# Kernel optimization log

Hardware: AMD Instinct MI355X
Metric: run time of the kernel (lower is better)

## Reference

```python
import jax, jax.numpy as jnp
import numpy as np

# ---- static config (mirrors init_kwargs) ----
NS, NV, ORDER = 16, 4, 1
NUM_RBF, NUM_CH = 8, 4
C = NUM_RBF * NUM_CH              # 32 output channels per l in out_irreps
N_NODES, N_EDGES = 10000, 128000
NODE_FEAT, EDGE_FEAT = 64, 16
RDIM, RMAX = 32, 12.0
L, FC_DIM = 2, 64
# FullyConnectedTensorProduct weight numel for order=1 paths:
# (0x0->0), (0x1->1), (1x0->1), (1x1->0), (1x1->1)
WNUM = NS*NS + NS*NV + NV*NV + NV*NS + NV*NV  # 416


def _get_sorter(order, nc):
    # faithful port of TensorProductConvModel.get_sorter
    idx, orl = [], []
    for l in range(order + 1):
        for n in range(nc):
            idx.extend([n] * (2 * l + 1))
            orl.extend(range(l * l, (l + 1) * (l + 1)))
    idx, orl = np.array(idx), np.array(orl)
    return np.argsort(idx * (orl.max() + 1) + orl, kind='stable')

SORTER = jnp.asarray(_get_sorter(ORDER, C))


def _mlp(x, W1, b1, W2, b2):
    return jnp.maximum(x @ W1 + b1, 0.0) @ W2 + b2


def setup_inputs() -> dict:
    key = jax.random.key(0)
    ks = jax.random.split(key, 24)
    rn = lambda k, sh, sc: jax.random.normal(k, sh, dtype=jnp.float32) * sc
    s = lambda f: 1.0 / np.sqrt(f)
    inp = {}
    inp['pos'] = rn(ks[0], (N_NODES, 3), 3.0)
    inp['node_feats'] = rn(ks[1], (N_NODES, NODE_FEAT), 1.0)
    inp['edge_attr_in'] = rn(ks[2], (N_EDGES, EDGE_FEAT), 1.0)
    inp['edge_index'] = jax.random.randint(ks[3], (2, N_EDGES), 0, N_NODES)
    # Encoder (linear) + node_embedding MLP
    inp['enc_W'] = rn(ks[4], (NODE_FEAT, NS), s(NODE_FEAT)); inp['enc_b'] = jnp.zeros((NS,), jnp.float32)
    inp['ne_W1'] = rn(ks[5], (NS, NS), s(NS)); inp['ne_b1'] = jnp.zeros((NS,), jnp.float32)
    inp['ne_W2'] = rn(ks[6], (NS, NS), s(NS)); inp['ne_b2'] = jnp.zeros((NS,), jnp.float32)
    # edge_embedding MLP
    inp['ee_W1'] = rn(ks[7], (EDGE_FEAT, NS), s(EDGE_FEAT)); inp['ee_b1'] = jnp.zeros((NS,), jnp.float32)
    inp['ee_W2'] = rn(ks[8], (NS, NS), s(NS)); inp['ee_b2'] = jnp.zeros((NS,), jnp.float32)
    # radius_embedding MLP
    inp['re_W1'] = rn(ks[9], (RDIM, NS), s(RDIM)); inp['re_b1'] = jnp.zeros((NS,), jnp.float32)
    inp['re_W2'] = rn(ks[10], (NS, NS), s(NS)); inp['re_b2'] = jnp.zeros((NS,), jnp.float32)
    # per-layer TP edge-weight MLPs (stacked over L layers)
    inp['fc1_W'] = rn(ks[11], (L, 3 * NS, FC_DIM), s(3 * NS)); inp['fc1_b'] = jnp.zeros((L, FC_DIM), jnp.float32)
    inp['fc2_W'] = rn(ks[12], (L, FC_DIM, WNUM), s(FC_DIM)); inp['fc2_b'] = jnp.zeros((L, WNUM), jnp.float32)
    # final o3.Linear (per-l channel mixing)
    inp['lin0_W'] = rn(ks[13], (NS, C), 1.0)
    inp['lin1_W'] = rn(ks[14], (NV, C), 1.0)
    return inp


def _forward(pos, node_feats, edge_attr_in, enc_W, enc_b, ne_W1, ne_b1, ne_W2, ne_b2,
             ee_W1, ee_b1, ee_W2, ee_b2, re_W1, re_b1, re_W2, re_b2,
             fc1_W, fc1_b, fc2_W, fc2_b, lin0_W, lin1_W, edge_index):
    src, dst = edge_index[0], edge_index[1]
    N, E = pos.shape[0], src.shape[0]
    # node scalar features: Encoder -> node_embedding MLP
    h0 = _mlp(node_feats @ enc_W + enc_b, ne_W1, ne_b1, ne_W2, ne_b2)        # [N, ns]
    h1 = jnp.zeros((N, NV, 3), h0.dtype)                                      # l=1 part (zero-padded)
    # build_conv_graph (radius=False): given edges only
    edge_vec = pos[src] - pos[dst]                                            # [E, 3]
    d = jnp.linalg.norm(edge_vec, axis=-1)
    offset = jnp.linspace(0.0, RMAX, RDIM)
    coeff = -0.5 / (offset[1] - offset[0]) ** 2
    rbf = jnp.exp(coeff * (d[:, None] - offset[None, :]) ** 2)                # GaussianSmearing
    edge_attr = _mlp(edge_attr_in, ee_W1, ee_b1, ee_W2, ee_b2) + _mlp(rbf, re_W1, re_b1, re_W2, re_b2)
    # spherical harmonics, normalize=True, component normalization: Y0=1, Y1=sqrt(3)*unit
    unit = edge_vec / jnp.maximum(d, 1e-9)[:, None]
    y1 = jnp.sqrt(3.0) * unit                                                 # [E, 3]
    # scatter-mean denominators (dim_size = N)
    cnt = jnp.maximum(jax.ops.segment_sum(jnp.ones((E,), h0.dtype), src, num_segments=N), 1.0)
    a0 = 1.0 / jnp.sqrt(float(NS + NV))       # path (fan-in) norm for l=0 output
    a1 = 1.0 / jnp.sqrt(float(NS + 2 * NV))   # path norm for l=1 output
    for i in range(L):
        # edge features: [edge_attr | h0[src] | h0[dst]] -> per-edge TP weights
        ea = jnp.concatenate([edge_attr, h0[src], h0[dst]], -1)
        w = _mlp(ea, fc1_W[i], fc1_b[i], fc2_W[i], fc2_b[i])                  # [E, WNUM]
        off = 0
        w00 = w[:, off:off + NS * NS].reshape(E, NS, NS); off += NS * NS
        w011 = w[:, off:off + NS * NV].reshape(E, NS, NV); off += NS * NV
        w101 = w[:, off:off + NV * NV].reshape(E, NV, NV); off += NV * NV
        w110 = w[:, off:off + NV * NS].reshape(E, NV, NS); off += NV * NS
        w111 = w[:, off:off + NV * NV].reshape(E, NV, NV)
        x0, x1 = h0[dst], h1[dst]                                             # gather at edge_dst
        # l=0 output: (0x0->0) + (1x1->0)
        dot = jnp.einsum('enk,ek->en', x1, y1) / jnp.sqrt(3.0)
        o0 = a0 * (jnp.einsum('en,eno->eo', x0, w00) + jnp.einsum('en,eno->eo', dot, w110))
        # l=1 output: (0x1->1) + (1x0->1) + (1x1->1 cross)
        cr = jnp.cross(x1, y1[:, None, :]) / jnp.sqrt(2.0)                    # [E, nv, 3]
        o1 = a1 * (jnp.einsum('en,eno,em->eom', x0, w011, y1)
                   + jnp.einsum('enm,eno->eom', x1, w101)
                   + jnp.einsum('enm,eno->eom', cr, w111))
        # scatter-mean into edge_src, residual add
        h0 = h0 + jax.ops.segment_sum(o0, src, num_segments=N) / cnt[:, None]
        h1 = h1 + jax.ops.segment_sum(o1.reshape(E, -1), src, num_segments=N).reshape(N, NV, 3) / cnt[:, None, None]
    # final o3.Linear (per-l, fan-in normalized) -> sorter -> reshape
    f0 = (h0 @ lin0_W) / jnp.sqrt(float(NS))                                   # [N, C]
    f1 = jnp.einsum('nvm,vc->ncm', h1, lin1_W) / jnp.sqrt(float(NV))           # [N, C, 3]
    flat = jnp.concatenate([f0, f1.reshape(N, C * 3)], -1)                     # irreps-flat layout
    return flat[:, SORTER].reshape(N, NUM_CH, NUM_RBF, (ORDER + 1) ** 2)


def reference(pos, node_feats, edge_attr_in, edge_index, enc_W, enc_b, ne_W1, ne_b1, ne_W2, ne_b2,
              ee_W1, ee_b1, ee_W2, ee_b2, re_W1, re_b1, re_W2, re_b2,
              fc1_W, fc1_b, fc2_W, fc2_b, lin0_W, lin1_W):
    return _forward(pos, node_feats, edge_attr_in, enc_W, enc_b, ne_W1, ne_b1, ne_W2, ne_b2,
                    ee_W1, ee_b1, ee_W2, ee_b2, re_W1, re_b1, re_W2, re_b2,
                    fc1_W, fc1_b, fc2_W, fc2_b, lin0_W, lin1_W, edge_index)
```

## Files before the change

kernel.cpp:

```cpp
#include <hip/hip_runtime.h>
#include <math.h>

#define SQRT3f     1.7320508075688772f
#define INV_SQRT3f 0.5773502691896258f
#define INV_SQRT2f 0.7071067811865476f
#define A0f        0.22360679774997896f
#define A1f        0.20412414523193150f

typedef __attribute__((ext_vector_type(8))) short bf16x8;
typedef __attribute__((ext_vector_type(4))) float f32x4;

__device__ __forceinline__ float4 ld4(const float* p) {
    return *reinterpret_cast<const float4*>(p);
}

__device__ __forceinline__ unsigned short f2bf(float x) {
    unsigned int u = __float_as_uint(x);
    u = (u + 0x7FFFu + ((u >> 16) & 1u)) >> 16;
    return (unsigned short)u;
}
__device__ __forceinline__ float bf2f(unsigned short u) {
    return __uint_as_float(((unsigned int)u) << 16);
}
__device__ __forceinline__ unsigned int pk2(float a, float b) {
    return (unsigned int)f2bf(a) | ((unsigned int)f2bf(b) << 16);
}

template<bool RELU>
__device__ __forceinline__ void mm16x16(const float* in, const float* W,
                                        const float* b, float* out)
{
#pragma unroll
    for (int t = 0; t < 16; ++t) out[t] = b[t];
#pragma unroll
    for (int s = 0; s < 16; ++s) {
        float a = in[s];
#pragma unroll
        for (int q = 0; q < 4; ++q) {
            float4 w = *reinterpret_cast<const float4*>(W + s * 16 + q * 4);
            out[q*4+0] += a * w.x; out[q*4+1] += a * w.y;
            out[q*4+2] += a * w.z; out[q*4+3] += a * w.w;
        }
    }
    if (RELU) {
#pragma unroll
        for (int t = 0; t < 16; ++t) out[t] = fmaxf(out[t], 0.f);
    }
}

__global__ __launch_bounds__(256)
void node_embed_kernel(const float* __restrict__ nf,
                       const float* __restrict__ encW, const float* __restrict__ encb,
                       const float* __restrict__ neW1, const float* __restrict__ neb1,
                       const float* __restrict__ neW2, const float* __restrict__ neb2,
                       float* __restrict__ h0, int N)
{
    int n = blockIdx.x * blockDim.x + threadIdx.x;
    if (n >= N) return;
    float x[16];
#pragma unroll
    for (int s = 0; s < 16; ++s) x[s] = encb[s];
    for (int i = 0; i < 64; ++i) {
        float a = nf[n * 64 + i];
#pragma unroll
        for (int q = 0; q < 4; ++q) {
            float4 w = ld4(encW + i * 16 + q * 4);
            x[q*4+0] += a * w.x; x[q*4+1] += a * w.y;
            x[q*4+2] += a * w.z; x[q*4+3] += a * w.w;
        }
    }
    float h[16], o[16];
    mm16x16<true >(x, neW1, neb1, h);
    mm16x16<false>(h, neW2, neb2, o);
#pragma unroll
    for (int j = 0; j < 16; ++j) h0[n * 16 + j] = o[j];
}

__global__ __launch_bounds__(256)
void hist_kernel(const int* __restrict__ srcI, int* __restrict__ cntI, int E)
{
    int e = blockIdx.x * blockDim.x + threadIdx.x;
    if (e < E) atomicAdd(&cntI[srcI[e]], 1);
}

__global__ __launch_bounds__(1024)
void scan_kernel(const int* __restrict__ cntI, int* __restrict__ start,
                 int* __restrict__ cursor, float* __restrict__ invcnt, int N)
{
    __shared__ int sd[1024];
    int tid = threadIdx.x;
    int run = 0;
    for (int c0 = 0; c0 < N; c0 += 1024) {
        int i = c0 + tid;
        int v = (i < N) ? cntI[i] : 0;
        sd[tid] = v;
        __syncthreads();
        for (int s = 1; s < 1024; s <<= 1) {
            int t = (tid >= s) ? sd[tid - s] : 0;
            __syncthreads();
            sd[tid] += t;
            __syncthreads();
        }
        int incl = sd[tid];
        int total = sd[1023];
        if (i < N) {
            int st = run + incl - v;
            start[i] = st;
            cursor[i] = st;
            invcnt[i] = 1.0f / fmaxf((float)v, 1.0f);
        }
        run += total;
        __syncthreads();
    }
}

__global__ __launch_bounds__(256)
void perm_kernel(const int* __restrict__ srcI, int* __restrict__ cursor,
                 int* __restrict__ perm, int E)
{
    int e = blockIdx.x * blockDim.x + threadIdx.x;
    if (e >= E) return;
    int p = atomicAdd(&cursor[srcI[e]], 1);
    perm[p] = e;
}

__global__ __launch_bounds__(256)
void edge_pre_kernel(const float* __restrict__ pos, const float* __restrict__ eain,
                     const int* __restrict__ srcI, const int* __restrict__ dstI,
                     const int* __restrict__ perm,
                     const float* __restrict__ eeW1, const float* __restrict__ eeb1,
                     const float* __restrict__ eeW2, const float* __restrict__ eeb2,
                     const float* __restrict__ reW1, const float* __restrict__ reb1,
                     const float* __restrict__ reW2, const float* __restrict__ reb2,
                     float* __restrict__ eattr, float* __restrict__ y1s,
                     int* __restrict__ srcS, int* __restrict__ dstS, int E)
{
    __shared__ float ws_[256 + 256 + 512 + 256];
    __shared__ float bs_[64];
    float* eeW1s = ws_;
    float* eeW2s = ws_ + 256;
    float* reW1s = ws_ + 512;
    float* reW2s = ws_ + 1024;
    int tid = threadIdx.x;
    if (tid < 256) eeW1s[tid] = eeW1[tid];
    if (tid < 256) eeW2s[tid] = eeW2[tid];
    for (int i = tid; i < 512; i += 256) reW1s[i] = reW1[i];
    if (tid < 256) reW2s[tid] = reW2[tid];
    if (tid < 16) bs_[tid]      = eeb1[tid];
    if (tid >= 16 && tid < 32)  bs_[tid] = eeb2[tid - 16];
    if (tid >= 32 && tid < 48)  bs_[tid] = reb1[tid - 32];
    if (tid >= 48 && tid < 64)  bs_[tid] = reb2[tid - 48];
    __syncthreads();

    int p = blockIdx.x * blockDim.x + tid;
    if (p >= E) return;
    int e = perm[p];
    int s = srcI[e], d = dstI[e];
    srcS[p] = s; dstS[p] = d;
    float vx = pos[s*3+0] - pos[d*3+0];
    float vy = pos[s*3+1] - pos[d*3+1];
    float vz = pos[s*3+2] - pos[d*3+2];
    float dist = sqrtf(vx*vx + vy*vy + vz*vz);
    float inv = 1.f / fmaxf(dist, 1e-9f);
    y1s[p*3+0] = SQRT3f * vx * inv;
    y1s[p*3+1] = SQRT3f * vy * inv;
    y1s[p*3+2] = SQRT3f * vz * inv;

    const float step  = 12.0f / 31.0f;
    const float coeff = -0.5f / (step * step);
    float rbf[32];
#pragma unroll
    for (int j = 0; j < 32; ++j) {
        float t = dist - (float)j * step;
        rbf[j] = expf(coeff * t * t);
    }

    float ein[16];
#pragma unroll
    for (int j = 0; j < 16; ++j) ein[j] = eain[(size_t)e * 16 + j];

    float t1[16], a1v[16];
    mm16x16<true >(ein, eeW1s, bs_, t1);
    mm16x16<false>(t1, eeW2s, bs_ + 16, a1v);

    float t2[16];
#pragma unroll
    for (int t = 0; t < 16; ++t) t2[t] = bs_[32 + t];
#pragma unroll
    for (int j = 0; j < 32; ++j) {
        float a = rbf[j];
#pragma unroll
        for (int q = 0; q < 4; ++q) {
            float4 w = *reinterpret_cast<const float4*>(&reW1s[j * 16 + q * 4]);
            t2[q*4+0] += a * w.x; t2[q*4+1] += a * w.y;
            t2[q*4+2] += a * w.z; t2[q*4+3] += a * w.w;
        }
    }
#pragma unroll
    for (int t = 0; t < 16; ++t) t2[t] = fmaxf(t2[t], 0.f);
    float a2v[16];
    mm16x16<false>(t2, reW2s, bs_ + 48, a2v);

#pragma unroll
    for (int j = 0; j < 16; ++j) eattr[(size_t)p * 16 + j] = a1v[j] + a2v[j];
}

__global__ void pack_w2_kernel(const float* __restrict__ fc2W, unsigned short* __restrict__ w2p)
{
    int idx = blockIdx.x * blockDim.x + threadIdx.x;
    if (idx >= 2 * 26 * 2 * 64) return;
    int lane  = idx & 63;
    int ks    = (idx >> 6) & 1;
    int nt    = (idx >> 7) % 26;
    int layer = idx / (26 * 2 * 64);
    const float* W = fc2W + (size_t)layer * 64 * 416;
    unsigned short* out = w2p + (size_t)layer * 26 * 2 * 64 * 8
                              + (size_t)((nt * 2 + ks) * 64 + lane) * 8;
    int k0 = ks * 32 + (lane >> 4) * 8;
    int c  = nt * 16 + (lane & 15);
#pragma unroll
    for (int j = 0; j < 8; ++j) out[j] = f2bf(W[(size_t)(k0 + j) * 416 + c]);
}

__global__ void pack_w1_kernel(const float* __restrict__ fc1W, unsigned short* __restrict__ w1p)
{
    int idx = blockIdx.x * blockDim.x + threadIdx.x;
    if (idx >= 2 * 4 * 2 * 64) return;
    int lane  = idx & 63;
    int ks    = (idx >> 6) & 1;
    int nt    = (idx >> 7) & 3;
    int layer = idx >> 9;
    const float* W = fc1W + (size_t)layer * 48 * 64;
    unsigned short* out = w1p + (size_t)(((layer * 4 + nt) * 2 + ks) * 64 + lane) * 8;
    int k0 = ks * 32 + (lane >> 4) * 8;
    int n  = nt * 16 + (lane & 15);
#pragma unroll
    for (int j = 0; j < 8; ++j) {
        int k = k0 + j;
        out[j] = (k < 48) ? f2bf(W[(size_t)k * 64 + n]) : (unsigned short)0;
    }
}

template<bool HAS_L1>
__global__ __launch_bounds__(256)
void fused_tp_kernel(const float* __restrict__ h0, const float* __restrict__ h1,
                     const float* __restrict__ eattr, const float* __restrict__ y1s,
                     const int* __restrict__ srcS, const int* __restrict__ dstS,
                     const unsigned short* __restrict__ w1p, const float* __restrict__ b1,
                     const unsigned short* __restrict__ w2p, const float* __restrict__ b2,
                     float* __restrict__ oo0, float* __restrict__ oo1, int E)
{
    __shared__ unsigned short eas[128 * 64];
    __shared__ unsigned short x0s[128 * 18];
    __shared__ unsigned short x1s[128 * 14];
    __shared__ unsigned short dots[128 * 6];
    __shared__ unsigned short crs[128 * 14];
    __shared__ unsigned short y1l[128 * 6];

    int tid = threadIdx.x;
    int ebase = blockIdx.x * 128;

    {
        int lx = tid & 127;
        int half = tid >> 7;
        int p = ebase + lx;
        int sw = lx & 7;
        uint4 pk;
        if (half == 0) {
            float4 va = ld4(eattr + (size_t)p * 16 + 0);
            float4 vb = ld4(eattr + (size_t)p * 16 + 4);
            float4 vc = ld4(eattr + (size_t)p * 16 + 8);
            float4 vd = ld4(eattr + (size_t)p * 16 + 12);
            pk.x = pk2(va.x, va.y); pk.y = pk2(va.z, va.w);
            pk.z = pk2(vb.x, vb.y); pk.w = pk2(vb.z, vb.w);
            *reinterpret_cast<uint4*>(&eas[lx * 64 + ((0 ^ sw) << 3)]) = pk;
            pk.x = pk2(vc.x, vc.y); pk.y = pk2(vc.z, vc.w);
            pk.z = pk2(vd.x, vd.y); pk.w = pk2(vd.z, vd.w);
            *reinterpret_cast<uint4*>(&eas[lx * 64 + ((1 ^ sw) << 3)]) = pk;

            int s = srcS[p];
            va = ld4(h0 + (size_t)s * 16 + 0); vb = ld4(h0 + (size_t)s * 16 + 4);
            vc = ld4(h0 + (size_t)s * 16 + 8); vd = ld4(h0 + (size_t)s * 16 + 12);
            pk.x = pk2(va.x, va.y); pk.y = pk2(va.z, va.w);
            pk.z = pk2(vb.x, vb.y); pk.w = pk2(vb.z, vb.w);
            *reinterpret_cast<uint4*>(&eas[lx * 64 + ((2 ^ sw) << 3)]) = pk;
            pk.x = pk2(vc.x, vc.y); pk.y = pk2(vc.z, vc.w);
            pk.z = pk2(vd.x, vd.y); pk.w = pk2(vd.z, vd.w);
            *reinterpret_cast<uint4*>(&eas[lx * 64 + ((3 ^ sw) << 3)]) = pk;
        } else {
            int d = dstS[p];
            float4 va = ld4(h0 + (size_t)d * 16 + 0);
            float4 vb = ld4(h0 + (size_t)d * 16 + 4);
            float4 vc = ld4(h0 + (size_t)d * 16 + 8);
            float4 vd = ld4(h0 + (size_t)d * 16 + 12);
            pk.x = pk2(va.x, va.y); pk.y = pk2(va.z, va.w);
            pk.z = pk2(vb.x, vb.y); pk.w = pk2(vb.z, vb.w);
            *reinterpret_cast<uint4*>(&eas[lx * 64 + ((4 ^ sw) << 3)]) = pk;
            pk.x = pk2(vc.x, vc.y); pk.y = pk2(vc.z, vc.w);
            pk.z = pk2(vd.x, vd.y); pk.w = pk2(vd.z, vd.w);
            *reinterpret_cast<uint4*>(&eas[lx * 64 + ((5 ^ sw) << 3)]) = pk;
            uint4 z = {0u, 0u, 0u, 0u};
            *reinterpret_cast<uint4*>(&eas[lx * 64 + ((6 ^ sw) << 3)]) = z;
            *reinterpret_cast<uint4*>(&eas[lx * 64 + ((7 ^ sw) << 3)]) = z;

            x0s[lx*18+ 0]=f2bf(va.x); x0s[lx*18+ 1]=f2bf(va.y);
            x0s[lx*18+ 2]=f2bf(va.z); x0s[lx*18+ 3]=f2bf(va.w);
            x0s[lx*18+ 4]=f2bf(vb.x); x0s[lx*18+ 5]=f2bf(vb.y);
            x0s[lx*18+ 6]=f2bf(vb.z); x0s[lx*18+ 7]=f2bf(vb.w);
            x0s[lx*18+ 8]=f2bf(vc.x); x0s[lx*18+ 9]=f2bf(vc.y);
            x0s[lx*18+10]=f2bf(vc.z); x0s[lx*18+11]=f2bf(vc.w);
            x0s[lx*18+12]=f2bf(vd.x); x0s[lx*18+13]=f2bf(vd.y);
            x0s[lx*18+14]=f2bf(vd.z); x0s[lx*18+15]=f2bf(vd.w);

            float yv0 = y1s[(size_t)p*3+0], yv1 = y1s[(size_t)p*3+1], yv2 = y1s[(size_t)p*3+2];
            y1l[lx*6+0] = f2bf(yv0); y1l[lx*6+1] = f2bf(yv1); y1l[lx*6+2] = f2bf(yv2);

            if (HAS_L1) {
#pragma unroll
                for (int v = 0; v < 4; ++v) {
                    float xa = h1[(size_t)d*12 + v*3 + 0];
                    float xb = h1[(size_t)d*12 + v*3 + 1];
                    float xc = h1[(size_t)d*12 + v*3 + 2];
                    x1s[lx*14 + v*3 + 0] = f2bf(xa);
                    x1s[lx*14 + v*3 + 1] = f2bf(xb);
                    x1s[lx*14 + v*3 + 2] = f2bf(xc);
                    dots[lx*6 + v] = f2bf((xa*yv0 + xb*yv1 + xc*yv2) * INV_SQRT3f);
                    crs[lx*14 + v*3 + 0] = f2bf((xb*yv2 - xc*yv1) * INV_SQRT2f);
                    crs[lx*14 + v*3 + 1] = f2bf((xc*yv0 - xa*yv2) * INV_SQRT2f);
                    crs[lx*14 + v*3 + 2] = f2bf((xa*yv1 - xb*yv0) * INV_SQRT2f);
                }
            }
        }
    }
    __syncthreads();

    int wave = tid >> 6;
    int lane = tid & 63;
    int col = lane & 15;
    int grp = lane >> 4;
    int mrow0 = wave * 32;

    {
        bf16x8 a1[2][2];
#pragma unroll
        for (int m = 0; m < 2; ++m) {
            int row = mrow0 + m * 16 + col;
            int r7 = row & 7;
#pragma unroll
            for (int ks = 0; ks < 2; ++ks) {
                int kc = grp + ks * 4;
                a1[m][ks] = *reinterpret_cast<const bf16x8*>(
                    &eas[row * 64 + ((kc ^ r7) << 3)]);
            }
        }
        f32x4 hacc[4][2];
#pragma unroll
        for (int nt = 0; nt < 4; ++nt) {
            const bf16x8* bp = reinterpret_cast<const bf16x8*>(
                w1p + (size_t)((nt * 2) * 64 + lane) * 8);
            bf16x8 b0 = bp[0];
            bf16x8 b1f = bp[64];
            float bs = b1[nt * 16 + col];
            f32x4 cin = {bs, bs, bs, bs};
#pragma unroll
            for (int m = 0; m < 2; ++m) {
                f32x4 acc = cin;
                acc = __builtin_amdgcn_mfma_f32_16x16x32_bf16(a1[m][0], b0, acc, 0, 0, 0);
                acc = __builtin_amdgcn_mfma_f32_16x16x32_bf16(a1[m][1], b1f, acc, 0, 0, 0);
                hacc[nt][m] = acc;
            }
        }
#pragma unroll
        for (int nt = 0; nt < 4; ++nt) {
            int chunkbase = nt * 2 + (col >> 3);
            int cw = col & 7;
#pragma unroll
            for (int m = 0; m < 2; ++m) {
#pragma unroll
                for (int r = 0; r < 4; ++r) {
                    int edge = mrow0 + m * 16 + grp * 4 + r;
                    unsigned short hv = f2bf(fmaxf(hacc[nt][m][r], 0.f));
                    eas[edge * 64 + ((chunkbase ^ (edge & 7)) << 3) + cw] = hv;
                }
            }
        }
    }

    asm volatile("s_waitcnt lgkmcnt(0)" ::: "memory");
    __builtin_amdgcn_sched_barrier(0);

    bf16x8 a[2][2];
#pragma unroll
    for (int m = 0; m < 2; ++m) {
        int row = mrow0 + m * 16 + col;
        int r7 = row & 7;
        a[m][0] = *reinterpret_cast<const bf16x8*>(&eas[row * 64 + ((grp ^ r7) << 3)]);
        a[m][1] = *reinterpret_cast<const bf16x8*>(&eas[row * 64 + (((grp + 4) ^ r7) << 3)]);
    }

    float o0a[2][4];
    float t011p[2][4];
    float o1p[2][4][3];
#pragma unroll
    for (int m = 0; m < 2; ++m)
#pragma unroll
        for (int r = 0; r < 4; ++r) {
            o0a[m][r] = 0.f; t011p[m][r] = 0.f;
            o1p[m][r][0] = 0.f; o1p[m][r][1] = 0.f; o1p[m][r][2] = 0.f;
        }

    const int NT = HAS_L1 ? 26 : 20;
    for (int nt = 0; nt < NT; ++nt) {
        const bf16x8* bp = reinterpret_cast<const bf16x8*>(
            w2p + (size_t)(nt * 2 * 64 + lane) * 8);
        bf16x8 b0 = bp[0];
        bf16x8 b1f = bp[64];
        float bias = b2[nt * 16 + col];
        f32x4 cin = {bias, bias, bias, bias};
#pragma unroll
        for (int m = 0; m < 2; ++m) {
            f32x4 acc = cin;
            acc = __builtin_amdgcn_mfma_f32_16x16x32_bf16(a[m][0], b0, acc, 0, 0, 0);
            acc = __builtin_amdgcn_mfma_f32_16x16x32_bf16(a[m][1], b1f, acc, 0, 0, 0);
            int lx0 = mrow0 + m * 16 + grp * 4;
            if (nt < 16) {
#pragma unroll
                for (int r = 0; r < 4; ++r)
                    o0a[m][r] += bf2f(x0s[(lx0 + r) * 18 + nt]) * acc[r];
            } else if (nt < 20) {
                int n = (nt - 16) * 4 + (col >> 2);
#pragma unroll
                for (int r = 0; r < 4; ++r)
                    t011p[m][r] += bf2f(x0s[(lx0 + r) * 18 + n]) * acc[r];
            } else if (nt == 20) {
                int n = col >> 2;
#pragma unroll
                for (int r = 0; r < 4; ++r) {
#pragma unroll
                    for (int d = 0; d < 3; ++d)
                        o1p[m][r][d] += bf2f(x1s[(lx0 + r) * 14 + n * 3 + d]) * acc[r];
                }
            } else if (nt < 25) {
                int n = nt - 21;
#pragma unroll
                for (int r = 0; r < 4; ++r)
                    o0a[m][r] += bf2f(dots[(lx0 + r) * 6 + n]) * acc[r];
            } else {
                int n = col >> 2;
#pragma unroll
                for (int r = 0; r < 4; ++r) {
#pragma unroll
                    for (int d = 0; d < 3; ++d)
                        o1p[m][r][d] += bf2f(crs[(lx0 + r) * 14 + n * 3 + d]) * acc[r];
                }
            }
        }
    }

#pragma unroll
    for (int m = 0; m < 2; ++m) {
        int lx0 = mrow0 + m * 16 + grp * 4;
#pragma unroll
        for (int r = 0; r < 4; ++r) {
            int lx = lx0 + r;
            size_t e = (size_t)(ebase + lx);
            float t = t011p[m][r];
            t += __shfl_xor(t, 4);
            t += __shfl_xor(t, 8);
            float o1v[3];
#pragma unroll
            for (int d = 0; d < 3; ++d) {
                float v = o1p[m][r][d];
                v += __shfl_xor(v, 4);
                v += __shfl_xor(v, 8);
                o1v[d] = v + t * bf2f(y1l[lx * 6 + d]);
            }
            oo0[e * 16 + col] = A0f * o0a[m][r];
            if (col < 4) {
#pragma unroll
                for (int d = 0; d < 3; ++d)
                    oo1[e * 12 + col * 3 + d] = A1f * o1v[d];
            }
        }
    }
}

__global__ void node_update_kernel(float* __restrict__ h0, float* __restrict__ h1,
                                   const float* __restrict__ oo0, const float* __restrict__ oo1,
                                   const int* __restrict__ start, const int* __restrict__ cntI,
                                   const float* __restrict__ invcnt, int N)
{
    int j = threadIdx.x;
    int n = blockIdx.x * blockDim.y + threadIdx.y;
    if (n >= N || j >= 28) return;
    int p0 = start[n], p1 = p0 + cntI[n];
    float acc = 0.f;
    if (j < 16) {
        for (int p = p0; p < p1; ++p) acc += oo0[(size_t)p * 16 + j];
        h0[(size_t)n * 16 + j] += acc * invcnt[n];
    } else {
        int m = j - 16;
        for (int p = p0; p < p1; ++p) acc += oo1[(size_t)p * 12 + m];
        h1[(size_t)n * 12 + m] += acc * invcnt[n];
    }
}

__global__ __launch_bounds__(256)
void final_kernel(const float* __restrict__ h0, const float* __restrict__ h1,
                  const float* __restrict__ lin0, const float* __restrict__ lin1,
                  float* __restrict__ out, int N)
{
    int i = blockIdx.x * blockDim.x + threadIdx.x;
    if (i >= N * 32) return;
    int n = i >> 5, c = i & 31;
    float f0 = 0.f;
#pragma unroll
    for (int s = 0; s < 16; ++s) f0 += h0[n * 16 + s] * lin0[s * 32 + c];
    f0 *= 0.25f;
    float f1x = 0.f, f1y = 0.f, f1z = 0.f;
#pragma unroll
    for (int v = 0; v < 4; ++v) {
        float w = lin1[v * 32 + c];
        f1x += h1[n * 12 + v * 3 + 0] * w;
        f1y += h1[n * 12 + v * 3 + 1] * w;
        f1z += h1[n * 12 + v * 3 + 2] * w;
    }
    float4 r;
    r.x = f0;
    r.y = f1x * 0.5f;
    r.z = f1y * 0.5f;
    r.w = f1z * 0.5f;
    *reinterpret_cast<float4*>(out + (size_t)n * 128 + c * 4) = r;
}

extern "C" void kernel_launch(void* const* d_in, const int* in_sizes, int n_in,
                              void* d_out, int out_size, void* d_ws, size_t ws_size,
                              hipStream_t stream)
{
    const float* pos  = (const float*)d_in[0];
    const float* nf   = (const float*)d_in[1];
    const float* eain = (const float*)d_in[2];
    const int*   eidx = (const int*)  d_in[3];
    const float* encW = (const float*)d_in[4];
    const float* encb = (const float*)d_in[5];
    const float* neW1 = (const float*)d_in[6];
    const float* neb1 = (const float*)d_in[7];
    const float* neW2 = (const float*)d_in[8];
    const float* neb2 = (const float*)d_in[9];
    const float* eeW1 = (const float*)d_in[10];
    const float* eeb1 = (const float*)d_in[11];
    const float* eeW2 = (const float*)d_in[12];
    const float* eeb2 = (const float*)d_in[13];
    const float* reW1 = (const float*)d_in[14];
    const float* reb1 = (const float*)d_in[15];
    const float* reW2 = (const float*)d_in[16];
    const float* reb2 = (const float*)d_in[17];
    const float* fc1W = (const float*)d_in[18];
    const float* fc1b = (const float*)d_in[19];
    const float* fc2W = (const float*)d_in[20];
    const float* fc2b = (const float*)d_in[21];
    const float* lin0 = (const float*)d_in[22];
    const float* lin1 = (const float*)d_in[23];

    int N = in_sizes[0] / 3;
    int E = in_sizes[3] / 2;
    const int* srcI = eidx;
    const int* dstI = eidx + E;

    float* ws = (float*)d_ws;
    size_t o = 0;
    float* h0     = ws + o; o += (size_t)N * 16;
    float* h1     = ws + o; o += (size_t)N * 12;
    float* eat    = ws + o; o += (size_t)E * 16;
    float* y1s    = ws + o; o += (size_t)E * 3;
    float* oo0    = ws + o; o += (size_t)E * 16;
    float* oo1    = ws + o; o += (size_t)E * 12;
    float* invcnt = ws + o; o += (size_t)N;
    int* cntI   = (int*)(ws + o); o += (size_t)N;
    int* startA = (int*)(ws + o); o += (size_t)N;
    int* cursor = (int*)(ws + o); o += (size_t)N;
    int* perm   = (int*)(ws + o); o += (size_t)E;
    int* srcS   = (int*)(ws + o); o += (size_t)E;
    int* dstS   = (int*)(ws + o); o += (size_t)E;
    unsigned short* w2p = (unsigned short*)(ws + o); o += 2 * 26 * 2 * 64 * 8 / 2;
    unsigned short* w1p = (unsigned short*)(ws + o); o += 2 * 4 * 2 * 64 * 8 / 2;

    hipMemsetAsync(h1,   0, sizeof(float) * (size_t)N * 12, stream);
    hipMemsetAsync(cntI, 0, sizeof(int) * (size_t)N, stream);

    pack_w2_kernel<<<26, 256, 0, stream>>>(fc2W, w2p);
    pack_w1_kernel<<<4, 256, 0, stream>>>(fc1W, w1p);
    node_embed_kernel<<<(N + 255) / 256, 256, 0, stream>>>(
        nf, encW, encb, neW1, neb1, neW2, neb2, h0, N);

    hist_kernel<<<(E + 255) / 256, 256, 0, stream>>>(srcI, cntI, E);
    scan_kernel<<<1, 1024, 0, stream>>>(cntI, startA, cursor, invcnt, N);
    perm_kernel<<<(E + 255) / 256, 256, 0, stream>>>(srcI, cursor, perm, E);

    edge_pre_kernel<<<(E + 255) / 256, 256, 0, stream>>>(
        pos, eain, srcI, dstI, perm, eeW1, eeb1, eeW2, eeb2,
        reW1, reb1, reW2, reb2, eat, y1s, srcS, dstS, E);

    for (int i = 0; i < 2; ++i) {
        const float* fb1 = fc1b + (size_t)i * 64;
        const float* fb2 = fc2b + (size_t)i * 416;
        const unsigned short* w1pi = w1p + (size_t)i * 4 * 2 * 64 * 8;
        const unsigned short* w2pi = w2p + (size_t)i * 26 * 2 * 64 * 8;
        if (i == 0) {
            fused_tp_kernel<false><<<E / 128, 256, 0, stream>>>(
                h0, h1, eat, y1s, srcS, dstS, w1pi, fb1, w2pi, fb2, oo0, oo1, E);
        } else {
            fused_tp_kernel<true><<<E / 128, 256, 0, stream>>>(
                h0, h1, eat, y1s, srcS, dstS, w1pi, fb1, w2pi, fb2, oo0, oo1, E);
        }
        dim3 blk(32, 8);
        node_update_kernel<<<(N + 7) / 8, blk, 0, stream>>>(
            h0, h1, oo0, oo1, startA, cntI, invcnt, N);
    }

    final_kernel<<<((size_t)N * 32 + 255) / 256, 256, 0, stream>>>(
        h0, h1, lin0, lin1, (float*)d_out, N);
}
```

Baseline: 287.6 us.

## Fuse embed with histogram, perm into edge_pre, and final linear into node update

Merges several small launches: the node embedding and the edge histogram share one grid, both weight-pack kernels become one, the permutation kernel is folded into edge_pre via an atomic cursor, and the final linear is fused into the last node-update pass. The scan is replaced with wave shuffles, and node update now reads float4 vectors and stages weights in shared memory. This cuts launch count and the perm array traffic. In exchange the edge order within each segment becomes nondeterministic, and edge_pre now reads in original edge order.

Result: faster. 265.3 us (-7.8%).

```diff
diff --git a/kernel.cpp b/kernel.cpp
--- a/kernel.cpp
+++ b/kernel.cpp
@@ -49,85 +49,101 @@
 }
 
 __global__ __launch_bounds__(256)
-void node_embed_kernel(const float* __restrict__ nf,
+void embed_hist_kernel(const float* __restrict__ nf,
                        const float* __restrict__ encW, const float* __restrict__ encb,
                        const float* __restrict__ neW1, const float* __restrict__ neb1,
                        const float* __restrict__ neW2, const float* __restrict__ neb2,
-                       float* __restrict__ h0, int N)
-{
-    int n = blockIdx.x * blockDim.x + threadIdx.x;
+                       float* __restrict__ h0, int N,
+                       const int* __restrict__ srcI, int* __restrict__ cntI, int E,
+                       int nblkA)
+{
+    int tid = threadIdx.x;
+    if ((int)blockIdx.x >= nblkA) {
+        int e = ((int)blockIdx.x - nblkA) * 256 + tid;
+        if (e < E) atomicAdd(&cntI[srcI[e]], 1);
+        return;
+    }
+    __shared__ float encWs[1024];
+    __shared__ float neW1s[256];
+    __shared__ float neW2s[256];
+    __shared__ float bs[48];
+    for (int i = tid; i < 1024; i += 256) encWs[i] = encW[i];
+    neW1s[tid] = neW1[tid];
+    neW2s[tid] = neW2[tid];
+    if (tid < 16)      bs[tid] = encb[tid];
+    else if (tid < 32) bs[tid] = neb1[tid - 16];
+    else if (tid < 48) bs[tid] = neb2[tid - 32];
+    __syncthreads();
+
+    int n = blockIdx.x * 256 + tid;
     if (n >= N) return;
     float x[16];
 #pragma unroll
-    for (int s = 0; s < 16; ++s) x[s] = encb[s];
+    for (int s = 0; s < 16; ++s) x[s] = bs[s];
     for (int i = 0; i < 64; ++i) {
-        float a = nf[n * 64 + i];
+        float a = nf[(size_t)n * 64 + i];
 #pragma unroll
         for (int q = 0; q < 4; ++q) {
-            float4 w = ld4(encW + i * 16 + q * 4);
+            float4 w = *reinterpret_cast<const float4*>(&encWs[i * 16 + q * 4]);
             x[q*4+0] += a * w.x; x[q*4+1] += a * w.y;
             x[q*4+2] += a * w.z; x[q*4+3] += a * w.w;
         }
     }
     float h[16], o[16];
-    mm16x16<true >(x, neW1, neb1, h);
-    mm16x16<false>(h, neW2, neb2, o);
-#pragma unroll
-    for (int j = 0; j < 16; ++j) h0[n * 16 + j] = o[j];
-}
-
-__global__ __launch_bounds__(256)
-void hist_kernel(const int* __restrict__ srcI, int* __restrict__ cntI, int E)
-{
-    int e = blockIdx.x * blockDim.x + threadIdx.x;
-    if (e < E) atomicAdd(&cntI[srcI[e]], 1);
+    mm16x16<true >(x, neW1s, bs + 16, h);
+    mm16x16<false>(h, neW2s, bs + 32, o);
+#pragma unroll
+    for (int j = 0; j < 16; ++j) h0[(size_t)n * 16 + j] = o[j];
 }
 
 __global__ __launch_bounds__(1024)
 void scan_kernel(const int* __restrict__ cntI, int* __restrict__ start,
                  int* __restrict__ cursor, float* __restrict__ invcnt, int N)
 {
-    __shared__ int sd[1024];
+    __shared__ int wsum[16];
+    __shared__ int ctot;
     int tid = threadIdx.x;
+    int lane = tid & 63, wid = tid >> 6;
     int run = 0;
     for (int c0 = 0; c0 < N; c0 += 1024) {
         int i = c0 + tid;
         int v = (i < N) ? cntI[i] : 0;
-        sd[tid] = v;
+        int x = v;
+#pragma unroll
+        for (int off = 1; off < 64; off <<= 1) {
+            int y = __shfl_up(x, off);
+            if (lane >= off) x += y;
+        }
+        if (lane == 63) wsum[wid] = x;
         __syncthreads();
-        for (int s = 1; s < 1024; s <<= 1) {
-            int t = (tid >= s) ? sd[tid - s] : 0;
-            __syncthreads();
-            sd[tid] += t;
-            __syncthreads();
-        }
-        int incl = sd[tid];
-        int total = sd[1023];
+        if (wid == 0) {
+            int w = (lane < 16) ? wsum[lane] : 0;
+#pragma unroll
+            for (int off = 1; off < 16; off <<= 1) {
+                int y = __shfl_up(w, off);
+                if (lane >= off) w += y;
+            }
+            if (lane < 16) wsum[lane] = w;
+            if (lane == 15) ctot = w;
+        }
+        __syncthreads();
+        int base = (wid > 0) ? wsum[wid - 1] : 0;
+        int incl = x + base;
         if (i < N) {
             int st = run + incl - v;
             start[i] = st;
             cursor[i] = st;
             invcnt[i] = 1.0f / fmaxf((float)v, 1.0f);
         }
-        run += total;
+        run += ctot;
         __syncthreads();
     }
-}
-
-__global__ __launch_bounds__(256)
-void perm_kernel(const int* __restrict__ srcI, int* __restrict__ cursor,
-                 int* __restrict__ perm, int E)
-{
-    int e = blockIdx.x * blockDim.x + threadIdx.x;
-    if (e >= E) return;
-    int p = atomicAdd(&cursor[srcI[e]], 1);
-    perm[p] = e;
 }
 
 __global__ __launch_bounds__(256)
 void edge_pre_kernel(const float* __restrict__ pos, const float* __restrict__ eain,
                      const int* __restrict__ srcI, const int* __restrict__ dstI,
-                     const int* __restrict__ perm,
+                     int* __restrict__ cursor,
                      const float* __restrict__ eeW1, const float* __restrict__ eeb1,
                      const float* __restrict__ eeW2, const float* __restrict__ eeb2,
                      const float* __restrict__ reW1, const float* __restrict__ reb1,
@@ -135,36 +151,37 @@
                      float* __restrict__ eattr, float* __restrict__ y1s,
                      int* __restrict__ srcS, int* __restrict__ dstS, int E)
 {
-    __shared__ float ws_[256 + 256 + 512 + 256];
+    __shared__ float ws_[1280];
     __shared__ float bs_[64];
     float* eeW1s = ws_;
     float* eeW2s = ws_ + 256;
     float* reW1s = ws_ + 512;
     float* reW2s = ws_ + 1024;
     int tid = threadIdx.x;
-    if (tid < 256) eeW1s[tid] = eeW1[tid];
-    if (tid < 256) eeW2s[tid] = eeW2[tid];
-    for (int i = tid; i < 512; i += 256) reW1s[i] = reW1[i];
-    if (tid < 256) reW2s[tid] = reW2[tid];
-    if (tid < 16) bs_[tid]      = eeb1[tid];
-    if (tid >= 16 && tid < 32)  bs_[tid] = eeb2[tid - 16];
-    if (tid >= 32 && tid < 48)  bs_[tid] = reb1[tid - 32];
-    if (tid >= 48 && tid < 64)  bs_[tid] = reb2[tid - 48];
+    eeW1s[tid] = eeW1[tid];
+    eeW2s[tid] = eeW2[tid];
+    reW1s[tid] = reW1[tid];
+    reW1s[tid + 256] = reW1[tid + 256];
+    reW2s[tid] = reW2[tid];
+    if (tid < 16)      bs_[tid] = eeb1[tid];
+    else if (tid < 32) bs_[tid] = eeb2[tid - 16];
+    else if (tid < 48) bs_[tid] = reb1[tid - 32];
+    else if (tid < 64) bs_[tid] = reb2[tid - 48];
     __syncthreads();
 
-    int p = blockIdx.x * blockDim.x + tid;
-    if (p >= E) return;
-    int e = perm[p];
+    int e = blockIdx.x * blockDim.x + tid;
+    if (e >= E) return;
     int s = srcI[e], d = dstI[e];
+    int p = atomicAdd(&cursor[s], 1);
     srcS[p] = s; dstS[p] = d;
     float vx = pos[s*3+0] - pos[d*3+0];
     float vy = pos[s*3+1] - pos[d*3+1];
     float vz = pos[s*3+2] - pos[d*3+2];
     float dist = sqrtf(vx*vx + vy*vy + vz*vz);
     float inv = 1.f / fmaxf(dist, 1e-9f);
-    y1s[p*3+0] = SQRT3f * vx * inv;
-    y1s[p*3+1] = SQRT3f * vy * inv;
-    y1s[p*3+2] = SQRT3f * vz * inv;
+    y1s[(size_t)p*3+0] = SQRT3f * vx * inv;
+    y1s[(size_t)p*3+1] = SQRT3f * vy * inv;
+    y1s[(size_t)p*3+2] = SQRT3f * vz * inv;
 
     const float step  = 12.0f / 31.0f;
     const float coeff = -0.5f / (step * step);
@@ -205,39 +222,39 @@
     for (int j = 0; j < 16; ++j) eattr[(size_t)p * 16 + j] = a1v[j] + a2v[j];
 }
 
-__global__ void pack_w2_kernel(const float* __restrict__ fc2W, unsigned short* __restrict__ w2p)
+__global__ void pack_w_kernel(const float* __restrict__ fc2W, const float* __restrict__ fc1W,
+                              unsigned short* __restrict__ w2p, unsigned short* __restrict__ w1p)
 {
     int idx = blockIdx.x * blockDim.x + threadIdx.x;
-    if (idx >= 2 * 26 * 2 * 64) return;
-    int lane  = idx & 63;
-    int ks    = (idx >> 6) & 1;
-    int nt    = (idx >> 7) % 26;
-    int layer = idx / (26 * 2 * 64);
-    const float* W = fc2W + (size_t)layer * 64 * 416;
-    unsigned short* out = w2p + (size_t)layer * 26 * 2 * 64 * 8
-                              + (size_t)((nt * 2 + ks) * 64 + lane) * 8;
-    int k0 = ks * 32 + (lane >> 4) * 8;
-    int c  = nt * 16 + (lane & 15);
-#pragma unroll
-    for (int j = 0; j < 8; ++j) out[j] = f2bf(W[(size_t)(k0 + j) * 416 + c]);
-}
-
-__global__ void pack_w1_kernel(const float* __restrict__ fc1W, unsigned short* __restrict__ w1p)
-{
-    int idx = blockIdx.x * blockDim.x + threadIdx.x;
-    if (idx >= 2 * 4 * 2 * 64) return;
-    int lane  = idx & 63;
-    int ks    = (idx >> 6) & 1;
-    int nt    = (idx >> 7) & 3;
-    int layer = idx >> 9;
-    const float* W = fc1W + (size_t)layer * 48 * 64;
-    unsigned short* out = w1p + (size_t)(((layer * 4 + nt) * 2 + ks) * 64 + lane) * 8;
-    int k0 = ks * 32 + (lane >> 4) * 8;
-    int n  = nt * 16 + (lane & 15);
-#pragma unroll
-    for (int j = 0; j < 8; ++j) {
-        int k = k0 + j;
-        out[j] = (k < 48) ? f2bf(W[(size_t)k * 64 + n]) : (unsigned short)0;
+    const int NW2 = 2 * 26 * 2 * 64;
+    if (idx < NW2) {
+        int lane  = idx & 63;
+        int ks    = (idx >> 6) & 1;
+        int nt    = (idx >> 7) % 26;
+        int layer = idx / (26 * 2 * 64);
+        const float* W = fc2W + (size_t)layer * 64 * 416;
+        unsigned short* out = w2p + (size_t)layer * 26 * 2 * 64 * 8
+                                  + (size_t)((nt * 2 + ks) * 64 + lane) * 8;
+        int k0 = ks * 32 + (lane >> 4) * 8;
+        int c  = nt * 16 + (lane & 15);
+#pragma unroll
+        for (int j = 0; j < 8; ++j) out[j] = f2bf(W[(size_t)(k0 + j) * 416 + c]);
+    } else {
+        int i2 = idx - NW2;
+        if (i2 >= 2 * 4 * 2 * 64) return;
+        int lane  = i2 & 63;
+        int ks    = (i2 >> 6) & 1;
+        int nt    = (i2 >> 7) & 3;
+        int layer = i2 >> 9;
+        const float* W = fc1W + (size_t)layer * 48 * 64;
+        unsigned short* out = w1p + (size_t)(((layer * 4 + nt) * 2 + ks) * 64 + lane) * 8;
+        int k0 = ks * 32 + (lane >> 4) * 8;
+        int n  = nt * 16 + (lane & 15);
+#pragma unroll
+        for (int j = 0; j < 8; ++j) {
+            int k = k0 + j;
+            out[j] = (k < 48) ? f2bf(W[(size_t)k * 64 + n]) : (unsigned short)0;
+        }
     }
 }
 
@@ -485,52 +502,92 @@
     }
 }
 
-__global__ void node_update_kernel(float* __restrict__ h0, float* __restrict__ h1,
-                                   const float* __restrict__ oo0, const float* __restrict__ oo1,
-                                   const int* __restrict__ start, const int* __restrict__ cntI,
-                                   const float* __restrict__ invcnt, int N)
-{
-    int j = threadIdx.x;
-    int n = blockIdx.x * blockDim.y + threadIdx.y;
-    if (n >= N || j >= 28) return;
-    int p0 = start[n], p1 = p0 + cntI[n];
-    float acc = 0.f;
-    if (j < 16) {
-        for (int p = p0; p < p1; ++p) acc += oo0[(size_t)p * 16 + j];
-        h0[(size_t)n * 16 + j] += acc * invcnt[n];
-    } else {
-        int m = j - 16;
-        for (int p = p0; p < p1; ++p) acc += oo1[(size_t)p * 12 + m];
-        h1[(size_t)n * 12 + m] += acc * invcnt[n];
-    }
-}
-
+template<bool FINAL>
 __global__ __launch_bounds__(256)
-void final_kernel(const float* __restrict__ h0, const float* __restrict__ h1,
-                  const float* __restrict__ lin0, const float* __restrict__ lin1,
-                  float* __restrict__ out, int N)
-{
-    int i = blockIdx.x * blockDim.x + threadIdx.x;
-    if (i >= N * 32) return;
-    int n = i >> 5, c = i & 31;
-    float f0 = 0.f;
-#pragma unroll
-    for (int s = 0; s < 16; ++s) f0 += h0[n * 16 + s] * lin0[s * 32 + c];
-    f0 *= 0.25f;
-    float f1x = 0.f, f1y = 0.f, f1z = 0.f;
-#pragma unroll
-    for (int v = 0; v < 4; ++v) {
-        float w = lin1[v * 32 + c];
-        f1x += h1[n * 12 + v * 3 + 0] * w;
-        f1y += h1[n * 12 + v * 3 + 1] * w;
-        f1z += h1[n * 12 + v * 3 + 2] * w;
-    }
-    float4 r;
-    r.x = f0;
-    r.y = f1x * 0.5f;
-    r.z = f1y * 0.5f;
-    r.w = f1z * 0.5f;
-    *reinterpret_cast<float4*>(out + (size_t)n * 128 + c * 4) = r;
+void node_update_kernel(float* __restrict__ h0, float* __restrict__ h1,
+                        const float* __restrict__ oo0, const float* __restrict__ oo1,
+                        const int* __restrict__ start, const int* __restrict__ cntI,
+                        const float* __restrict__ invcnt,
+                        const float* __restrict__ lin0, const float* __restrict__ lin1,
+                        float* __restrict__ out, int N)
+{
+    __shared__ float lin0s[512];
+    __shared__ float lin1s[128];
+    __shared__ float hh0[32][16];
+    __shared__ float hh1[32][12];
+
+    int tx = threadIdx.x;
+    int ty = threadIdx.y;
+    int tid = ty * 8 + tx;
+    if (FINAL) {
+        lin0s[tid] = lin0[tid];
+        lin0s[tid + 256] = lin0[tid + 256];
+        if (tid < 128) lin1s[tid] = lin1[tid];
+    }
+
+    int n = blockIdx.x * 32 + ty;
+    if (n < N) {
+        int p0 = start[n], c = cntI[n];
+        float4 acc = {0.f, 0.f, 0.f, 0.f};
+        if (tx < 4) {
+            for (int k = 0; k < c; ++k) {
+                float4 v = ld4(oo0 + (size_t)(p0 + k) * 16 + tx * 4);
+                acc.x += v.x; acc.y += v.y; acc.z += v.z; acc.w += v.w;
+            }
+        } else if (tx < 7) {
+            for (int k = 0; k < c; ++k) {
+                float4 v = ld4(oo1 + (size_t)(p0 + k) * 12 + (tx - 4) * 4);
+                acc.x += v.x; acc.y += v.y; acc.z += v.z; acc.w += v.w;
+            }
+        }
+        float invc = invcnt[n];
+        if (tx < 4) {
+            float4 h = ld4(h0 + (size_t)n * 16 + tx * 4);
+            h.x += acc.x * invc; h.y += acc.y * invc;
+            h.z += acc.z * invc; h.w += acc.w * invc;
+            if (FINAL) {
+                hh0[ty][tx*4+0] = h.x; hh0[ty][tx*4+1] = h.y;
+                hh0[ty][tx*4+2] = h.z; hh0[ty][tx*4+3] = h.w;
+            } else {
+                *reinterpret_cast<float4*>(h0 + (size_t)n * 16 + tx * 4) = h;
+            }
+        } else if (tx < 7) {
+            float4 h = ld4(h1 + (size_t)n * 12 + (tx - 4) * 4);
+            h.x += acc.x * invc; h.y += acc.y * invc;
+            h.z += acc.z * invc; h.w += acc.w * invc;
+            if (FINAL) {
+                hh1[ty][(tx-4)*4+0] = h.x; hh1[ty][(tx-4)*4+1] = h.y;
+                hh1[ty][(tx-4)*4+2] = h.z; hh1[ty][(tx-4)*4+3] = h.w;
+            } else {
+                *reinterpret_cast<float4*>(h1 + (size_t)n * 12 + (tx - 4) * 4) = h;
+            }
+        }
+    }
+    if (FINAL) {
+        __syncthreads();
+        if (n >= N) return;
+#pragma unroll
+        for (int q = 0; q < 4; ++q) {
+            int c = tx * 4 + q;
+            float f0 = 0.f;
+#pragma unroll
+            for (int s = 0; s < 16; ++s) f0 += hh0[ty][s] * lin0s[s * 32 + c];
+            float f1x = 0.f, f1y = 0.f, f1z = 0.f;
+#pragma unroll
+            for (int v = 0; v < 4; ++v) {
+                float w = lin1s[v * 32 + c];
+                f1x += hh1[ty][v * 3 + 0] * w;
+                f1y += hh1[ty][v * 3 + 1] * w;
+                f1z += hh1[ty][v * 3 + 2] * w;
+            }
+            float4 r;
+            r.x = f0 * 0.25f;
+            r.y = f1x * 0.5f;
+            r.z = f1y * 0.5f;
+            r.w = f1z * 0.5f;
+            *reinterpret_cast<float4*>(out + (size_t)n * 128 + c * 4) = r;
+        }
+    }
 }
 
 extern "C" void kernel_launch(void* const* d_in, const int* in_sizes, int n_in,
@@ -579,7 +636,6 @@
     int* cntI   = (int*)(ws + o); o += (size_t)N;
     int* startA = (int*)(ws + o); o += (size_t)N;
     int* cursor = (int*)(ws + o); o += (size_t)N;
-    int* perm   = (int*)(ws + o); o += (size_t)E;
     int* srcS   = (int*)(ws + o); o += (size_t)E;
     int* dstS   = (int*)(ws + o); o += (size_t)E;
     unsigned short* w2p = (unsigned short*)(ws + o); o += 2 * 26 * 2 * 64 * 8 / 2;
@@ -588,19 +644,21 @@
     hipMemsetAsync(h1,   0, sizeof(float) * (size_t)N * 12, stream);
     hipMemsetAsync(cntI, 0, sizeof(int) * (size_t)N, stream);
 
-    pack_w2_kernel<<<26, 256, 0, stream>>>(fc2W, w2p);
-    pack_w1_kernel<<<4, 256, 0, stream>>>(fc1W, w1p);
-    node_embed_kernel<<<(N + 255) / 256, 256, 0, stream>>>(
-        nf, encW, encb, neW1, neb1, neW2, neb2, h0, N);
-
-    hist_kernel<<<(E + 255) / 256, 256, 0, stream>>>(srcI, cntI, E);
+    pack_w_kernel<<<30, 256, 0, stream>>>(fc2W, fc1W, w2p, w1p);
+
+    int nblkA = (N + 255) / 256;
+    int nblkB = (E + 255) / 256;
+    embed_hist_kernel<<<nblkA + nblkB, 256, 0, stream>>>(
+        nf, encW, encb, neW1, neb1, neW2, neb2, h0, N, srcI, cntI, E, nblkA);
+
     scan_kernel<<<1, 1024, 0, stream>>>(cntI, startA, cursor, invcnt, N);
-    perm_kernel<<<(E + 255) / 256, 256, 0, stream>>>(srcI, cursor, perm, E);
-
-    edge_pre_kernel<<<(E + 255) / 256, 256, 0, stream>>>(
-        pos, eain, srcI, dstI, perm, eeW1, eeb1, eeW2, eeb2,
+
+    edge_pre_kernel<<<nblkB, 256, 0, stream>>>(
+        pos, eain, srcI, dstI, cursor, eeW1, eeb1, eeW2, eeb2,
         reW1, reb1, reW2, reb2, eat, y1s, srcS, dstS, E);
 
+    dim3 nub(8, 32);
+    int nublk = (N + 31) / 32;
     for (int i = 0; i < 2; ++i) {
         const float* fb1 = fc1b + (size_t)i * 64;
         const float* fb2 = fc2b + (size_t)i * 416;
@@ -609,15 +667,13 @@
         if (i == 0) {
             fused_tp_kernel<false><<<E / 128, 256, 0, stream>>>(
                 h0, h1, eat, y1s, srcS, dstS, w1pi, fb1, w2pi, fb2, oo0, oo1, E);
+            node_update_kernel<false><<<nublk, nub, 0, stream>>>(
+                h0, h1, oo0, oo1, startA, cntI, invcnt, lin0, lin1, (float*)d_out, N);
         } else {
             fused_tp_kernel<true><<<E / 128, 256, 0, stream>>>(
                 h0, h1, eat, y1s, srcS, dstS, w1pi, fb1, w2pi, fb2, oo0, oo1, E);
-        }
-        dim3 blk(32, 8);
-        node_update_kernel<<<(N + 7) / 8, blk, 0, stream>>>(
-            h0, h1, oo0, oo1, startA, cntI, invcnt, N);
-    }
-
-    final_kernel<<<((size_t)N * 32 + 255) / 256, 256, 0, stream>>>(
-        h0, h1, lin0, lin1, (float*)d_out, N);
-}
+            node_update_kernel<true><<<nublk, nub, 0, stream>>>(
+                h0, h1, oo0, oo1, startA, cntI, invcnt, lin0, lin1, (float*)d_out, N);
+        }
+    }
+}
```
